# Kernel tuning notes

Measured on AMD Instinct MI355X. Metric: run time of the kernel, lower is better.

Reference implementation:

```python
import jax, jax.numpy as jnp
import numpy as np

D = 128
H = 4
L = 3
MAX_LEN = 696


def _pe(max_len, d):
    pos = jnp.arange(max_len, dtype=jnp.float32)[:, None]
    div = jnp.exp(jnp.arange(0, d, 2, dtype=jnp.float32) * (-jnp.log(jnp.float32(10000.0)) / d))
    pe = jnp.zeros((max_len, d), dtype=jnp.float32)
    pe = pe.at[:, 0::2].set(jnp.sin(pos * div))
    pe = pe.at[:, 1::2].set(jnp.cos(pos * div))
    return pe  # [max_len, d]


def _ln(x, w, b, eps=1e-5):
    m = jnp.mean(x, axis=-1, keepdims=True)
    v = jnp.mean((x - m) ** 2, axis=-1, keepdims=True)
    return (x - m) / jnp.sqrt(v + eps) * w + b


def _mha(xq, xkv, wqkv, bqkv, wo, bo, mask=None):
    # xq: [Tq,B,d], xkv: [Tk,B,d] (seq-first, torch convention)
    d = xq.shape[-1]
    hd = d // H
    q = xq @ wqkv[:d].T + bqkv[:d]
    k = xkv @ wqkv[d:2 * d].T + bqkv[d:2 * d]
    v = xkv @ wqkv[2 * d:].T + bqkv[2 * d:]

    def split(t):
        T, B, _ = t.shape
        return t.reshape(T, B, H, hd).transpose(1, 2, 0, 3)  # [B,H,T,hd]

    qh, kh, vh = split(q), split(k), split(v)
    s = jnp.einsum('bhqd,bhkd->bhqk', qh, kh) / jnp.sqrt(jnp.float32(hd))
    if mask is not None:
        s = jnp.where(mask, jnp.float32(-1e9), s)
    a = jax.nn.softmax(s, axis=-1)
    o = jnp.einsum('bhqk,bhkd->bhqd', a, vh)
    Tq, B = xq.shape[0], xq.shape[1]
    o = o.transpose(2, 0, 1, 3).reshape(Tq, B, d)
    return o @ wo.T + bo


def _forward(src, tgt, emb_in_w, emb_in_b, emb_out_w, emb_out_b,
             enc_qkv_w, enc_qkv_b, enc_proj_w, enc_proj_b,
             enc_ff1_w, enc_ff1_b, enc_ff2_w, enc_ff2_b, enc_ln_w, enc_ln_b,
             dec_sa_qkv_w, dec_sa_qkv_b, dec_sa_proj_w, dec_sa_proj_b,
             dec_ca_qkv_w, dec_ca_qkv_b, dec_ca_proj_w, dec_ca_proj_b,
             dec_ff1_w, dec_ff1_b, dec_ff2_w, dec_ff2_b, dec_ln_w, dec_ln_b,
             head_w, head_b):
    pe = _pe(MAX_LEN, D)
    # ---- encoder ----
    src_p = jnp.transpose(src, (2, 0, 1))  # [S,B,1]
    x = src_p @ emb_in_w.T + emb_in_b + pe[:src_p.shape[0], None, :]
    for i in range(L):
        a = _mha(x, x, enc_qkv_w[i], enc_qkv_b[i], enc_proj_w[i], enc_proj_b[i])
        x = _ln(x + a, enc_ln_w[i, 0], enc_ln_b[i, 0])
        f = jax.nn.relu(x @ enc_ff1_w[i].T + enc_ff1_b[i]) @ enc_ff2_w[i].T + enc_ff2_b[i]
        x = _ln(x + f, enc_ln_w[i, 1], enc_ln_b[i, 1])
    memory = x  # [S,B,D]
    # ---- decoder (full teacher forcing: loop collapses to one causal pass) ----
    tgt_p = jnp.transpose(tgt, (2, 0, 1))  # [T,B,1]
    T = tgt_p.shape[0]
    y = tgt_p[:T - 1] @ emb_out_w.T + emb_out_b  # [T-1,B,D]
    # original code applies pos encoding only to the initial token of the decode loop
    y = y.at[0].add(pe[0])
    mask = jnp.triu(jnp.ones((T - 1, T - 1), dtype=bool), k=1)  # True = masked
    for i in range(L):
        a = _mha(y, y, dec_sa_qkv_w[i], dec_sa_qkv_b[i], dec_sa_proj_w[i], dec_sa_proj_b[i], mask=mask)
        y = _ln(y + a, dec_ln_w[i, 0], dec_ln_b[i, 0])
        c = _mha(y, memory, dec_ca_qkv_w[i], dec_ca_qkv_b[i], dec_ca_proj_w[i], dec_ca_proj_b[i])
        y = _ln(y + c, dec_ln_w[i, 1], dec_ln_b[i, 1])
        f = jax.nn.relu(y @ dec_ff1_w[i].T + dec_ff1_b[i]) @ dec_ff2_w[i].T + dec_ff2_b[i]
        y = _ln(y + f, dec_ln_w[i, 2], dec_ln_b[i, 2])
    out = y @ head_w.T + head_b  # [T-1,B,1]
    return jnp.transpose(out, (1, 2, 0))  # [B,1,T-1]


def setup_inputs() -> dict:
    key = jax.random.key(0)
    ks = iter(jax.random.split(key, 64))

    def n(shape, s=0.02):
        return (jax.random.normal(next(ks), shape) * s).astype(jnp.float32)

    return {
        'src': jax.random.normal(next(ks), (64, 1, 696), dtype=jnp.float32),
        'tgt': jax.random.normal(next(ks), (64, 1, 512), dtype=jnp.float32),
        'emb_in_w': n((D, 1)), 'emb_in_b': n((D,)),
        'emb_out_w': n((D, 1)), 'emb_out_b': n((D,)),
        'enc_qkv_w': n((L, 3 * D, D)), 'enc_qkv_b': n((L, 3 * D)),
        'enc_proj_w': n((L, D, D)), 'enc_proj_b': n((L, D)),
        'enc_ff1_w': n((L, D, D)), 'enc_ff1_b': n((L, D)),
        'enc_ff2_w': n((L, D, D)), 'enc_ff2_b': n((L, D)),
        'enc_ln_w': jnp.ones((L, 2, D), dtype=jnp.float32),
        'enc_ln_b': jnp.zeros((L, 2, D), dtype=jnp.float32),
        'dec_sa_qkv_w': n((L, 3 * D, D)), 'dec_sa_qkv_b': n((L, 3 * D)),
        'dec_sa_proj_w': n((L, D, D)), 'dec_sa_proj_b': n((L, D)),
        'dec_ca_qkv_w': n((L, 3 * D, D)), 'dec_ca_qkv_b': n((L, 3 * D)),
        'dec_ca_proj_w': n((L, D, D)), 'dec_ca_proj_b': n((L, D)),
        'dec_ff1_w': n((L, D, D)), 'dec_ff1_b': n((L, D)),
        'dec_ff2_w': n((L, D, D)), 'dec_ff2_b': n((L, D)),
        'dec_ln_w': jnp.ones((L, 3, D), dtype=jnp.float32),
        'dec_ln_b': jnp.zeros((L, 3, D), dtype=jnp.float32),
        'head_w': n((1, D)), 'head_b': n((1,)),
    }


def reference(src, tgt, emb_in_w, emb_in_b, emb_out_w, emb_out_b,
              enc_qkv_w, enc_qkv_b, enc_proj_w, enc_proj_b,
              enc_ff1_w, enc_ff1_b, enc_ff2_w, enc_ff2_b, enc_ln_w, enc_ln_b,
              dec_sa_qkv_w, dec_sa_qkv_b, dec_sa_proj_w, dec_sa_proj_b,
              dec_ca_qkv_w, dec_ca_qkv_b, dec_ca_proj_w, dec_ca_proj_b,
              dec_ff1_w, dec_ff1_b, dec_ff2_w, dec_ff2_b, dec_ln_w, dec_ln_b,
              head_w, head_b):
    return _forward(src, tgt, emb_in_w, emb_in_b, emb_out_w, emb_out_b,
                    enc_qkv_w, enc_qkv_b, enc_proj_w, enc_proj_b,
                    enc_ff1_w, enc_ff1_b, enc_ff2_w, enc_ff2_b, enc_ln_w, enc_ln_b,
                    dec_sa_qkv_w, dec_sa_qkv_b, dec_sa_proj_w, dec_sa_proj_b,
                    dec_ca_qkv_w, dec_ca_qkv_b, dec_ca_proj_w, dec_ca_proj_b,
                    dec_ff1_w, dec_ff1_b, dec_ff2_w, dec_ff2_b, dec_ln_w, dec_ln_b,
                    head_w, head_b)
```

## Files before the change

kernel.cpp:

```cpp
#include <hip/hip_runtime.h>
#include <hip/hip_bf16.h>


typedef unsigned short u16;
typedef unsigned int u32;
typedef float f32x4 __attribute__((ext_vector_type(4)));
typedef float f32x2 __attribute__((ext_vector_type(2)));
typedef float f32x16 __attribute__((ext_vector_type(16)));
typedef unsigned short u16x8 __attribute__((ext_vector_type(8)));
typedef unsigned int u32x2 __attribute__((ext_vector_type(2)));
typedef unsigned int u32x4 __attribute__((ext_vector_type(4)));
typedef __bf16 bf16x8 __attribute__((ext_vector_type(8)));

static __device__ __forceinline__ float bf2f(u16 u) {
  u32 x = ((u32)u) << 16;
  return __builtin_bit_cast(float, x);
}
static __device__ __forceinline__ u16 f2bf(float f) {
  u32 x = __builtin_bit_cast(u32, f);
  u32 r = (x + 0x7fffu + ((x >> 16) & 1u)) >> 16;
  return (u16)r;
}
static __device__ __forceinline__ f32x4 mfma16(bf16x8 a, bf16x8 b, f32x4 c) {
  return __builtin_amdgcn_mfma_f32_16x16x32_bf16(a, b, c, 0, 0, 0);
}
static __device__ __forceinline__ f32x16 mfma32(bf16x8 a, bf16x8 b, f32x16 c) {
  return __builtin_amdgcn_mfma_f32_32x32x16_bf16(a, b, c, 0, 0, 0);
}
static __device__ __forceinline__ void plswap(u32& a, u32& b) {
  u32x2 r = __builtin_amdgcn_permlane32_swap(a, b, false, false);
  a = r.x; b = r.y;
}

__global__ void detect_k(const u32* __restrict__ ones, int* __restrict__ flag) {
  *flag = (ones[0] == 0x3F803F80u) ? 1 : 0;
}

struct CvtArgs {
  const void* p[32];
  int n[32];
  int off[32];
};

__global__ __launch_bounds__(256) void cvt_all(CvtArgs A, const int* __restrict__ flag,
                                               float* __restrict__ poolf,
                                               u16* __restrict__ poolb) {
  int ti = blockIdx.y;
  int i = blockIdx.x * 256 + threadIdx.x;
  int n = A.n[ti];
  if (i >= n) return;
  int o = A.off[ti] + i;
  if (*flag) {
    u16 raw = ((const u16*)A.p[ti])[i];
    poolb[o] = raw;
    poolf[o] = bf2f(raw);
  } else {
    float v = ((const float*)A.p[ti])[i];
    poolf[o] = v;
    poolb[o] = f2bf(v);
  }
}

__global__ void embed_enc(const float* __restrict__ src, const float* __restrict__ w,
                          const float* __restrict__ b, float* __restrict__ X,
                          u16* __restrict__ Xb) {
  int s = blockIdx.x, d = threadIdx.x;
  float freq = __expf(-(float)(d & 126) * 0.07195578415606394f);
  float arg = (float)s * freq;
  float pe = (d & 1) ? cosf(arg) : sinf(arg);
  float wd = w[d], bd = b[d];
  for (int bb = 0; bb < 64; ++bb) {
    float v = src[bb * 696 + s] * wd + bd + pe;
    size_t o = ((size_t)s * 64 + bb) * 128 + d;
    X[o] = v;
    Xb[o] = f2bf(v);
  }
}

__global__ void embed_dec(const float* __restrict__ tgt, const float* __restrict__ w,
                          const float* __restrict__ b, float* __restrict__ Y,
                          u16* __restrict__ Yb) {
  int tt = blockIdx.x, d = threadIdx.x;
  float wd = w[d], bd = b[d];
  float pe0 = (tt == 0 && (d & 1)) ? 1.0f : 0.0f;
  for (int bb = 0; bb < 64; ++bb) {
    float v = tgt[bb * 512 + tt] * wd + bd + pe0;
    size_t o = ((size_t)tt * 64 + bb) * 128 + d;
    Y[o] = v;
    Yb[o] = f2bf(v);
  }
}

__global__ __launch_bounds__(256) void gemm_ln(
    const u16* __restrict__ Xb, const u16* __restrict__ Wb,
    const float* __restrict__ bias, float* __restrict__ R,
    u16* __restrict__ Rb, const float* __restrict__ lnw,
    const float* __restrict__ lnb) {
  __shared__ u16 Ws[128][136];
  const int t = threadIdx.x;
  const int n0 = blockIdx.x << 6;
  const int wv = t >> 6, lane = t & 63, lg = lane >> 4, lr = lane & 15;
  const int r0 = n0 + (wv << 4);

#pragma unroll
  for (int i = 0; i < 8; ++i) {
    int idx = t + (i << 8);
    int r = idx >> 4, c = (idx & 15) << 3;
    *(u16x8*)&Ws[r][c] = *(const u16x8*)(Wb + ((size_t)r << 7) + c);
  }
  bf16x8 afr[4];
  const int arow = r0 + lr;
#pragma unroll
  for (int ks = 0; ks < 4; ++ks)
    afr[ks] = *(const bf16x8*)(Xb + ((size_t)arow << 7) + (ks << 5) + (lg << 3));
  __syncthreads();

  f32x4 acc[8] = {};
#pragma unroll
  for (int ks = 0; ks < 4; ++ks) {
#pragma unroll
    for (int cb = 0; cb < 8; ++cb) {
      bf16x8 bfr = *(const bf16x8*)&Ws[(cb << 4) + lr][(ks << 5) + (lg << 3)];
      acc[cb] = mfma16(afr[ks], bfr, acc[cb]);
    }
  }

  float vals[8][4];
#pragma unroll
  for (int cb = 0; cb < 8; ++cb) {
    float bv = bias[(cb << 4) + lr];
#pragma unroll
    for (int r = 0; r < 4; ++r) {
      size_t row = (size_t)(r0 + (lg << 2) + r);
      vals[cb][r] = acc[cb][r] + bv + R[(row << 7) + (cb << 4) + lr];
    }
  }
  float mean[4], rstd[4];
#pragma unroll
  for (int r = 0; r < 4; ++r) {
    float s = 0.0f, s2 = 0.0f;
#pragma unroll
    for (int cb = 0; cb < 8; ++cb) {
      float v = vals[cb][r];
      s += v; s2 += v * v;
    }
    s += __shfl_xor(s, 1); s2 += __shfl_xor(s2, 1);
    s += __shfl_xor(s, 2); s2 += __shfl_xor(s2, 2);
    s += __shfl_xor(s, 4); s2 += __shfl_xor(s2, 4);
    s += __shfl_xor(s, 8); s2 += __shfl_xor(s2, 8);
    float m = s * 0.0078125f;
    float var = s2 * 0.0078125f - m * m;
    mean[r] = m;
    rstd[r] = rsqrtf(var + 1e-5f);
  }
#pragma unroll
  for (int cb = 0; cb < 8; ++cb) {
    float w = lnw[(cb << 4) + lr], bb = lnb[(cb << 4) + lr];
#pragma unroll
    for (int r = 0; r < 4; ++r) {
      float v = (vals[cb][r] - mean[r]) * rstd[r] * w + bb;
      size_t o = ((size_t)(r0 + (lg << 2) + r) << 7) + (cb << 4) + lr;
      R[o] = v;
      Rb[o] = f2bf(v);
    }
  }
}

__global__ __launch_bounds__(256) void gemm_ff(
    const u16* __restrict__ Xb, const u16* __restrict__ W1,
    const float* __restrict__ b1, const u16* __restrict__ W2,
    const float* __restrict__ b2, float* __restrict__ R,
    u16* __restrict__ Rb, const float* __restrict__ lnw,
    const float* __restrict__ lnb) {
  __shared__ u16 Ws[128][136];
  __shared__ u16 Hs[64][136];
  const int t = threadIdx.x;
  const int n0 = blockIdx.x << 6;
  const int wv = t >> 6, lane = t & 63, lg = lane >> 4, lr = lane & 15;
  const int r0 = n0 + (wv << 4);

#pragma unroll
  for (int i = 0; i < 8; ++i) {
    int idx = t + (i << 8);
    int r = idx >> 4, c = (idx & 15) << 3;
    *(u16x8*)&Ws[r][c] = *(const u16x8*)(W1 + ((size_t)r << 7) + c);
  }
  bf16x8 afr[4];
  const int arow = r0 + lr;
#pragma unroll
  for (int ks = 0; ks < 4; ++ks)
    afr[ks] = *(const bf16x8*)(Xb + ((size_t)arow << 7) + (ks << 5) + (lg << 3));
  __syncthreads();

  f32x4 acc[8] = {};
#pragma unroll
  for (int ks = 0; ks < 4; ++ks) {
#pragma unroll
    for (int cb = 0; cb < 8; ++cb) {
      bf16x8 bfr = *(const bf16x8*)&Ws[(cb << 4) + lr][(ks << 5) + (lg << 3)];
      acc[cb] = mfma16(afr[ks], bfr, acc[cb]);
    }
  }
#pragma unroll
  for (int cb = 0; cb < 8; ++cb) {
    float bv = b1[(cb << 4) + lr];
#pragma unroll
    for (int r = 0; r < 4; ++r) {
      float v = fmaxf(acc[cb][r] + bv, 0.0f);
      Hs[(wv << 4) + (lg << 2) + r][(cb << 4) + lr] = f2bf(v);
    }
  }
  __syncthreads();

#pragma unroll
  for (int i = 0; i < 8; ++i) {
    int idx = t + (i << 8);
    int r = idx >> 4, c = (idx & 15) << 3;
    *(u16x8*)&Ws[r][c] = *(const u16x8*)(W2 + ((size_t)r << 7) + c);
  }
  __syncthreads();

  bf16x8 hfr[4];
#pragma unroll
  for (int ks = 0; ks < 4; ++ks)
    hfr[ks] = *(const bf16x8*)&Hs[(wv << 4) + lr][(ks << 5) + (lg << 3)];
#pragma unroll
  for (int cb = 0; cb < 8; ++cb) acc[cb] = f32x4{0, 0, 0, 0};
#pragma unroll
  for (int ks = 0; ks < 4; ++ks) {
#pragma unroll
    for (int cb = 0; cb < 8; ++cb) {
      bf16x8 bfr = *(const bf16x8*)&Ws[(cb << 4) + lr][(ks << 5) + (lg << 3)];
      acc[cb] = mfma16(hfr[ks], bfr, acc[cb]);
    }
  }

  float vals[8][4];
#pragma unroll
  for (int cb = 0; cb < 8; ++cb) {
    float bv = b2[(cb << 4) + lr];
#pragma unroll
    for (int r = 0; r < 4; ++r) {
      size_t row = (size_t)(r0 + (lg << 2) + r);
      vals[cb][r] = acc[cb][r] + bv + R[(row << 7) + (cb << 4) + lr];
    }
  }
  float mean[4], rstd[4];
#pragma unroll
  for (int r = 0; r < 4; ++r) {
    float s = 0.0f, s2 = 0.0f;
#pragma unroll
    for (int cb = 0; cb < 8; ++cb) {
      float v = vals[cb][r];
      s += v; s2 += v * v;
    }
    s += __shfl_xor(s, 1); s2 += __shfl_xor(s2, 1);
    s += __shfl_xor(s, 2); s2 += __shfl_xor(s2, 2);
    s += __shfl_xor(s, 4); s2 += __shfl_xor(s2, 4);
    s += __shfl_xor(s, 8); s2 += __shfl_xor(s2, 8);
    float m = s * 0.0078125f;
    float var = s2 * 0.0078125f - m * m;
    mean[r] = m;
    rstd[r] = rsqrtf(var + 1e-5f);
  }
#pragma unroll
  for (int cb = 0; cb < 8; ++cb) {
    float w = lnw[(cb << 4) + lr], bb = lnb[(cb << 4) + lr];
#pragma unroll
    for (int r = 0; r < 4; ++r) {
      float v = (vals[cb][r] - mean[r]) * rstd[r] * w + bb;
      size_t o = ((size_t)(r0 + (lg << 2) + r) << 7) + (cb << 4) + lr;
      R[o] = v;
      Rb[o] = f2bf(v);
    }
  }
}

__global__ __launch_bounds__(256) void gemm_qkv(
    const u16* __restrict__ Xb, const u16* __restrict__ Wb,
    const float* __restrict__ bias, u16* __restrict__ Qg,
    u16* __restrict__ Kg, u16* __restrict__ Vg, int M, int kbase, int vbase) {
  __shared__ u16 Xs[64][136];
  __shared__ u16 Ws[64][136];
  const int t = threadIdx.x;
  const int n0 = blockIdx.x << 6, m0 = blockIdx.y << 6;
  const int wq = t >> 6, lane = t & 63, lg = lane >> 4, lr = lane & 15;
  const int wr = (wq >> 1) << 5, wc = (wq & 1) << 5;
  const float QS = 0.17677669529663687f * 1.4426950408889634f;

#pragma unroll
  for (int i = 0; i < 4; ++i) {
    int idx = t + (i << 8);
    int r = idx >> 4, c = (idx & 15) << 3;
    *(u16x8*)&Xs[r][c] = *(const u16x8*)(Xb + (size_t)(n0 + r) * 128 + c);
    *(u16x8*)&Ws[r][c] = *(const u16x8*)(Wb + (size_t)(m0 + r) * 128 + c);
  }
  __syncthreads();

  f32x4 acc00 = {0,0,0,0}, acc01 = {0,0,0,0}, acc10 = {0,0,0,0}, acc11 = {0,0,0,0};
#pragma unroll
  for (int ks = 0; ks < 4; ++ks) {
    bf16x8 a0 = *(const bf16x8*)&Xs[wr + lr][(ks << 5) + (lg << 3)];
    bf16x8 a1 = *(const bf16x8*)&Xs[wr + 16 + lr][(ks << 5) + (lg << 3)];
    bf16x8 b0 = *(const bf16x8*)&Ws[wc + lr][(ks << 5) + (lg << 3)];
    bf16x8 b1 = *(const bf16x8*)&Ws[wc + 16 + lr][(ks << 5) + (lg << 3)];
    acc00 = mfma16(a0, b0, acc00);
    acc01 = mfma16(a0, b1, acc01);
    acc10 = mfma16(a1, b0, acc10);
    acc11 = mfma16(a1, b1, acc11);
  }

  f32x4 accs[2][2] = {{acc00, acc01}, {acc10, acc11}};
#pragma unroll
  for (int mi = 0; mi < 2; ++mi) {
#pragma unroll
    for (int ni = 0; ni < 2; ++ni) {
      int col = m0 + wc + (ni << 4) + lr;
      float bv = bias[col];
#pragma unroll
      for (int r = 0; r < 4; ++r) {
        int row = n0 + wr + (mi << 4) + (lg << 2) + r;
        float v = accs[mi][ni][r] + bv;
        size_t ro = (size_t)row << 7;
        if (col < kbase) {
          Qg[ro + col] = f2bf(v * QS);
        } else if (col < vbase) {
          Kg[ro + (col - kbase)] = f2bf(v);
        } else {
          Vg[ro + (col - vbase)] = f2bf(v);
        }
      }
    }
  }
}

__global__ __launch_bounds__(256) void attn_g(
    const u16* __restrict__ Qg, const u16* __restrict__ Kg,
    const u16* __restrict__ Vg, u16* __restrict__ Ob,
    int Tq, int Tk, int causal, int bpb) {
  __shared__ u16 Ks[64][44];
  __shared__ u16 Vs[32][74];
  __shared__ float Lw[4][36];
  const int t = threadIdx.x;
  const int wv = t >> 6, lane = t & 63;
  const int lq = lane & 31, hi = lane >> 5;
  const int p = blockIdx.x;
  const int idx = p >> 3;
  const int bh = ((p & 7) << 5) + idx / bpb;
  const int blk = idx % bpb;
  const int nstrips = (Tq + 31) >> 5;
  const int strip = blk * 4 + wv;
  const bool active = strip < nstrips;
  const int b = bh >> 2, h = bh & 3;
  const int qw = (active ? strip : (nstrips - 1)) << 5;

  bf16x8 qf[2];
  {
    int ql = qw + lq; if (ql > Tq - 1) ql = Tq - 1;
    const u16* qp = Qg + (((size_t)ql * 64 + b) << 7) + h * 32 + (hi << 3);
    qf[0] = *(const bf16x8*)qp;
    qf[1] = *(const bf16x8*)(qp + 16);
  }

  f32x16 o = {};
  float lsum = 0.0f;

  const int nfull = causal ? (qw >> 6) : (Tk >> 6);
  int lastcol = causal ? qw + 31 : Tk - 1;
  if (lastcol > Tk - 1) lastcol = Tk - 1;
  int ntiles = (lastcol >> 6) + 1;
  if (!active) ntiles = 0;

  int lastq_blk = blk * 128 + 127;
  if (lastq_blk > Tq - 1) lastq_blk = Tq - 1;
  int lastcol_blk = causal ? lastq_blk : Tk - 1;
  if (lastcol_blk > Tk - 1) lastcol_blk = Tk - 1;
  const int ntb = (lastcol_blk >> 6) + 1;

  const int stok = t >> 2, sc = (t & 3) << 3;

  for (int kt = 0; kt < ntb; ++kt) {
    const int k0 = kt << 6;
    __syncthreads();
    {
      int tok = k0 + stok; if (tok > Tk - 1) tok = Tk - 1;
      size_t roff = (((size_t)tok * 64 + b) << 7) + h * 32 + sc;
      *(u16x8*)&Ks[stok][sc] = *(const u16x8*)(Kg + roff);
      u16x8 vv = *(const u16x8*)(Vg + roff);
#pragma unroll
      for (int e = 0; e < 8; ++e) Vs[sc + e][stok] = vv[e];
    }
    __syncthreads();
    if (kt >= ntiles) continue;
    const bool masked = (kt >= nfull);

#pragma unroll
    for (int kb = 0; kb < 2; ++kb) {
      const int krow = (kb << 5) + lq;
      bf16x8 ka0 = *(const bf16x8*)&Ks[krow][hi << 3];
      bf16x8 ka1 = *(const bf16x8*)&Ks[krow][16 + (hi << 3)];
      f32x16 s = {};
      __builtin_amdgcn_s_setprio(1);
      s = mfma32(ka0, qf[0], s);
      s = mfma32(ka1, qf[1], s);
      __builtin_amdgcn_s_setprio(0);

      float pv[16];
#pragma unroll
      for (int r = 0; r < 16; ++r) {
        float sv = s[r];
        if (masked) {
          int kk = k0 + (kb << 5) + (r & 3) + ((r >> 2) << 3) + (hi << 2);
          int q = qw + lq;
          bool ok = causal ? (kk <= q) : (kk < Tk);
          sv = ok ? sv : -1e30f;
        }
        float e = exp2f(sv);
        pv[r] = e;
        lsum += e;
      }
      u32 u[8];
#pragma unroll
      for (int m = 0; m < 8; ++m)
        asm("v_cvt_pk_bf16_f32 %0, %1, %2" : "=v"(u[m]) : "v"(pv[2 * m]), "v"(pv[2 * m + 1]));

#pragma unroll
      for (int c = 0; c < 2; ++c) {
        u32 a0 = u[4 * c + 0], b0 = u[4 * c + 2];
        u32 a1 = u[4 * c + 1], b1 = u[4 * c + 3];
        plswap(a0, b0);
        plswap(a1, b1);
        u32x4 wv4 = {a0, a1, b0, b1};
        bf16x8 pf = __builtin_bit_cast(bf16x8, wv4);
        bf16x8 vf = *(const bf16x8*)&Vs[lq][(kb << 5) + (c << 4) + (hi << 3)];
        __builtin_amdgcn_s_setprio(1);
        o = mfma32(pf, vf, o);
        __builtin_amdgcn_s_setprio(0);
      }
    }
  }

  if (active) {
    float lt = lsum + __shfl_xor(lsum, 32);
    if (hi == 0) Lw[wv][lq] = 1.0f / lt;
    f32x4 li[4];
#pragma unroll
    for (int g = 0; g < 4; ++g)
      li[g] = *(const f32x4*)&Lw[wv][(hi << 2) + (g << 3)];
#pragma unroll
    for (int r = 0; r < 16; ++r) {
      int q = qw + (r & 3) + ((r >> 2) << 3) + (hi << 2);
      if (q < Tq) {
        Ob[(((size_t)q * 64 + b) << 7) + h * 32 + lq] = f2bf(o[r] * li[r >> 2][r & 3]);
      }
    }
  }
}

__global__ __launch_bounds__(256) void head_k(
    const float* __restrict__ Y, const float* __restrict__ w,
    const float* __restrict__ bh, void* __restrict__ out, const int* __restrict__ flag) {
  int n = (blockIdx.x << 2) + (threadIdx.x >> 6);
  int lane = threadIdx.x & 63;
  const float* yp = Y + (size_t)n * 128 + (lane << 1);
  float s = yp[0] * w[lane << 1] + yp[1] * w[(lane << 1) + 1];
#pragma unroll
  for (int off = 1; off < 64; off <<= 1) s += __shfl_xor(s, off);
  if (lane == 0) {
    int tt = n >> 6, bb = n & 63;
    float r = s + bh[0];
    int idx = bb * 511 + tt;
    if (*flag) ((u16*)out)[idx] = f2bf(r);
    else       ((float*)out)[idx] = r;
  }
}

extern "C" void kernel_launch(void* const* d_in, const int* in_sizes, int n_in,
                              void* d_out, int out_size, void* d_ws, size_t ws_size,
                              hipStream_t stream) {
  (void)out_size; (void)ws_size;
  CvtArgs A;
  long off[33]; off[0] = 0;
  int maxn = 0;
  for (int i = 0; i < 32; ++i) {
    int n = (i < n_in) ? in_sizes[i] : 0;
    A.p[i] = (i < n_in) ? d_in[i] : d_in[0];
    A.n[i] = n;
    A.off[i] = (int)off[i];
    off[i + 1] = off[i] + n;
    if (n > maxn) maxn = n;
  }
  const size_t offA = (size_t)((off[32] + 15) & ~15l);

  const size_t NE = 44544;
  const size_t ND = 32704;
  float* ws   = (float*)d_ws;
  int*   flag = (int*)d_ws;
  float* Wp   = ws + 16;
  float* Xe   = Wp + offA;
  float* Yd   = Xe + NE * 128;
  u16*   U    = (u16*)(Yd + ND * 128);
  u16*   Wb   = U;
  u16*   Xebf = Wb + offA;
  u16*   Ydbf = Xebf + NE * 128;
  u16*   TMPbf= Ydbf + ND * 128;
  u16*   Qgb  = TMPbf + NE * 128;
  u16*   Kgb  = Qgb + NE * 128;
  u16*   Vgb  = Kgb + NE * 128;

  const float* F = Wp;
  detect_k<<<1, 1, 0, stream>>>((const u32*)d_in[14], flag);
  cvt_all<<<dim3((maxn + 255) / 256, 32), 256, 0, stream>>>(A, flag, Wp, Wb);

  embed_enc<<<dim3(696), dim3(128), 0, stream>>>(F + A.off[0], F + A.off[2], F + A.off[3], Xe, Xebf);
  for (int i = 0; i < 3; ++i) {
    gemm_qkv<<<dim3(696, 6), 256, 0, stream>>>(Xebf, Wb + A.off[6] + i * 49152, F + A.off[7] + i * 384,
                                               Qgb, Kgb, Vgb, 384, 128, 256);
    attn_g<<<dim3(1536), 256, 0, stream>>>(Qgb, Kgb, Vgb, TMPbf, 696, 696, 0, 6);
    gemm_ln<<<dim3(696), 256, 0, stream>>>(TMPbf, Wb + A.off[8] + i * 16384, F + A.off[9] + i * 128,
                                           Xe, Xebf, F + A.off[14] + (i * 2 + 0) * 128, F + A.off[15] + (i * 2 + 0) * 128);
    gemm_ff<<<dim3(696), 256, 0, stream>>>(Xebf, Wb + A.off[10] + i * 16384, F + A.off[11] + i * 128,
                                           Wb + A.off[12] + i * 16384, F + A.off[13] + i * 128,
                                           Xe, Xebf, F + A.off[14] + (i * 2 + 1) * 128, F + A.off[15] + (i * 2 + 1) * 128);
  }

  embed_dec<<<dim3(511), dim3(128), 0, stream>>>(F + A.off[1], F + A.off[4], F + A.off[5], Yd, Ydbf);
  for (int i = 0; i < 3; ++i) {
    gemm_qkv<<<dim3(511, 6), 256, 0, stream>>>(Ydbf, Wb + A.off[16] + i * 49152, F + A.off[17] + i * 384,
                                               Qgb, Kgb, Vgb, 384, 128, 256);
    attn_g<<<dim3(1024), 256, 0, stream>>>(Qgb, Kgb, Vgb, TMPbf, 511, 511, 1, 4);
    gemm_ln<<<dim3(511), 256, 0, stream>>>(TMPbf, Wb + A.off[18] + i * 16384, F + A.off[19] + i * 128,
                                           Yd, Ydbf, F + A.off[28] + (i * 3 + 0) * 128, F + A.off[29] + (i * 3 + 0) * 128);
    gemm_qkv<<<dim3(511, 2), 256, 0, stream>>>(Ydbf, Wb + A.off[20] + i * 49152, F + A.off[21] + i * 384,
                                               Qgb, nullptr, nullptr, 128, 128, 128);
    gemm_qkv<<<dim3(696, 4), 256, 0, stream>>>(Xebf, Wb + A.off[20] + i * 49152 + 16384, F + A.off[21] + i * 384 + 128,
                                               nullptr, Kgb, Vgb, 256, 0, 128);
    attn_g<<<dim3(1024), 256, 0, stream>>>(Qgb, Kgb, Vgb, TMPbf, 511, 696, 0, 4);
    gemm_ln<<<dim3(511), 256, 0, stream>>>(TMPbf, Wb + A.off[22] + i * 16384, F + A.off[23] + i * 128,
                                           Yd, Ydbf, F + A.off[28] + (i * 3 + 1) * 128, F + A.off[29] + (i * 3 + 1) * 128);
    gemm_ff<<<dim3(511), 256, 0, stream>>>(Ydbf, Wb + A.off[24] + i * 16384, F + A.off[25] + i * 128,
                                           Wb + A.off[26] + i * 16384, F + A.off[27] + i * 128,
                                           Yd, Ydbf, F + A.off[28] + (i * 3 + 2) * 128, F + A.off[29] + (i * 3 + 2) * 128);
  }

  head_k<<<dim3(8176), 256, 0, stream>>>(Yd, F + A.off[30], F + A.off[31], d_out, flag);
}
```

Before: 823.8 us.

## Fuse attention with output projection, residual add and LayerNorm

Replaces the separate attention and gemm_ln kernels with one kernel. Each block handles one batch element and a 64-query strip across all four heads, one head per wave. After normalising, the block writes the attention output to shared memory and runs the output projection, residual add and LayerNorm in place. This removes the bf16 intermediate round trip through global memory and one launch per attention layer. In exchange there are fewer blocks (704 and 512 instead of 1536 and 1024), larger shared-memory use and more work per block, which can lower occupancy and load balance, especially on the causal path.

```diff
diff --git a/kernel.cpp b/kernel.cpp
--- a/kernel.cpp
+++ b/kernel.cpp
@@ -91,81 +91,6 @@
   }
 }
 
-__global__ __launch_bounds__(256) void gemm_ln(
-    const u16* __restrict__ Xb, const u16* __restrict__ Wb,
-    const float* __restrict__ bias, float* __restrict__ R,
-    u16* __restrict__ Rb, const float* __restrict__ lnw,
-    const float* __restrict__ lnb) {
-  __shared__ u16 Ws[128][136];
-  const int t = threadIdx.x;
-  const int n0 = blockIdx.x << 6;
-  const int wv = t >> 6, lane = t & 63, lg = lane >> 4, lr = lane & 15;
-  const int r0 = n0 + (wv << 4);
-
-#pragma unroll
-  for (int i = 0; i < 8; ++i) {
-    int idx = t + (i << 8);
-    int r = idx >> 4, c = (idx & 15) << 3;
-    *(u16x8*)&Ws[r][c] = *(const u16x8*)(Wb + ((size_t)r << 7) + c);
-  }
-  bf16x8 afr[4];
-  const int arow = r0 + lr;
-#pragma unroll
-  for (int ks = 0; ks < 4; ++ks)
-    afr[ks] = *(const bf16x8*)(Xb + ((size_t)arow << 7) + (ks << 5) + (lg << 3));
-  __syncthreads();
-
-  f32x4 acc[8] = {};
-#pragma unroll
-  for (int ks = 0; ks < 4; ++ks) {
-#pragma unroll
-    for (int cb = 0; cb < 8; ++cb) {
-      bf16x8 bfr = *(const bf16x8*)&Ws[(cb << 4) + lr][(ks << 5) + (lg << 3)];
-      acc[cb] = mfma16(afr[ks], bfr, acc[cb]);
-    }
-  }
-
-  float vals[8][4];
-#pragma unroll
-  for (int cb = 0; cb < 8; ++cb) {
-    float bv = bias[(cb << 4) + lr];
-#pragma unroll
-    for (int r = 0; r < 4; ++r) {
-      size_t row = (size_t)(r0 + (lg << 2) + r);
-      vals[cb][r] = acc[cb][r] + bv + R[(row << 7) + (cb << 4) + lr];
-    }
-  }
-  float mean[4], rstd[4];
-#pragma unroll
-  for (int r = 0; r < 4; ++r) {
-    float s = 0.0f, s2 = 0.0f;
-#pragma unroll
-    for (int cb = 0; cb < 8; ++cb) {
-      float v = vals[cb][r];
-      s += v; s2 += v * v;
-    }
-    s += __shfl_xor(s, 1); s2 += __shfl_xor(s2, 1);
-    s += __shfl_xor(s, 2); s2 += __shfl_xor(s2, 2);
-    s += __shfl_xor(s, 4); s2 += __shfl_xor(s2, 4);
-    s += __shfl_xor(s, 8); s2 += __shfl_xor(s2, 8);
-    float m = s * 0.0078125f;
-    float var = s2 * 0.0078125f - m * m;
-    mean[r] = m;
-    rstd[r] = rsqrtf(var + 1e-5f);
-  }
-#pragma unroll
-  for (int cb = 0; cb < 8; ++cb) {
-    float w = lnw[(cb << 4) + lr], bb = lnb[(cb << 4) + lr];
-#pragma unroll
-    for (int r = 0; r < 4; ++r) {
-      float v = (vals[cb][r] - mean[r]) * rstd[r] * w + bb;
-      size_t o = ((size_t)(r0 + (lg << 2) + r) << 7) + (cb << 4) + lr;
-      R[o] = v;
-      Rb[o] = f2bf(v);
-    }
-  }
-}
-
 __global__ __launch_bounds__(256) void gemm_ff(
     const u16* __restrict__ Xb, const u16* __restrict__ W1,
     const float* __restrict__ b1, const u16* __restrict__ W2,
@@ -334,125 +259,197 @@
   }
 }
 
-__global__ __launch_bounds__(256) void attn_g(
+__global__ __launch_bounds__(256) void attn_pl(
     const u16* __restrict__ Qg, const u16* __restrict__ Kg,
-    const u16* __restrict__ Vg, u16* __restrict__ Ob,
-    int Tq, int Tk, int causal, int bpb) {
-  __shared__ u16 Ks[64][44];
-  __shared__ u16 Vs[32][74];
-  __shared__ float Lw[4][36];
+    const u16* __restrict__ Vg, const u16* __restrict__ Wp,
+    const float* __restrict__ bp, float* __restrict__ R,
+    u16* __restrict__ Rb, const float* __restrict__ lnw,
+    const float* __restrict__ lnb, int Tq, int Tk, int causal, int nstrips) {
+  __shared__ u16 KOs[64][132];
+  __shared__ u16 Vs[128][70];
+  __shared__ u16 Ws[64][132];
+  __shared__ float Lw[4][2][36];
   const int t = threadIdx.x;
   const int wv = t >> 6, lane = t & 63;
   const int lq = lane & 31, hi = lane >> 5;
+  const int lr16 = lane & 15, lg16 = lane >> 4;
+  const int h = wv;
   const int p = blockIdx.x;
   const int idx = p >> 3;
-  const int bh = ((p & 7) << 5) + idx / bpb;
-  const int blk = idx % bpb;
-  const int nstrips = (Tq + 31) >> 5;
-  const int strip = blk * 4 + wv;
-  const bool active = strip < nstrips;
-  const int b = bh >> 2, h = bh & 3;
-  const int qw = (active ? strip : (nstrips - 1)) << 5;
-
-  bf16x8 qf[2];
-  {
-    int ql = qw + lq; if (ql > Tq - 1) ql = Tq - 1;
+  const int b = ((p & 7) << 3) + idx / nstrips;
+  const int strip = idx % nstrips;
+  const int q0 = strip << 6;
+
+  bf16x8 qf[2][2];
+#pragma unroll
+  for (int ss = 0; ss < 2; ++ss) {
+    int ql = q0 + (ss << 5) + lq; if (ql > Tq - 1) ql = Tq - 1;
     const u16* qp = Qg + (((size_t)ql * 64 + b) << 7) + h * 32 + (hi << 3);
-    qf[0] = *(const bf16x8*)qp;
-    qf[1] = *(const bf16x8*)(qp + 16);
-  }
-
-  f32x16 o = {};
-  float lsum = 0.0f;
-
-  const int nfull = causal ? (qw >> 6) : (Tk >> 6);
-  int lastcol = causal ? qw + 31 : Tk - 1;
-  if (lastcol > Tk - 1) lastcol = Tk - 1;
-  int ntiles = (lastcol >> 6) + 1;
-  if (!active) ntiles = 0;
-
-  int lastq_blk = blk * 128 + 127;
-  if (lastq_blk > Tq - 1) lastq_blk = Tq - 1;
-  int lastcol_blk = causal ? lastq_blk : Tk - 1;
-  if (lastcol_blk > Tk - 1) lastcol_blk = Tk - 1;
-  const int ntb = (lastcol_blk >> 6) + 1;
-
-  const int stok = t >> 2, sc = (t & 3) << 3;
+    qf[ss][0] = *(const bf16x8*)qp;
+    qf[ss][1] = *(const bf16x8*)(qp + 16);
+  }
+
+  f32x16 o[2] = {};
+  float lsum[2] = {0.0f, 0.0f};
+
+  const int ntb = causal ? (strip + 1) : (((Tk - 1) >> 6) + 1);
 
   for (int kt = 0; kt < ntb; ++kt) {
     const int k0 = kt << 6;
     __syncthreads();
-    {
-      int tok = k0 + stok; if (tok > Tk - 1) tok = Tk - 1;
-      size_t roff = (((size_t)tok * 64 + b) << 7) + h * 32 + sc;
-      *(u16x8*)&Ks[stok][sc] = *(const u16x8*)(Kg + roff);
-      u16x8 vv = *(const u16x8*)(Vg + roff);
-#pragma unroll
-      for (int e = 0; e < 8; ++e) Vs[sc + e][stok] = vv[e];
+#pragma unroll
+    for (int i = 0; i < 4; ++i) {
+      int sidx = t + (i << 8);
+      int row = sidx >> 4, c8 = (sidx & 15) << 3;
+      int tok = k0 + row; if (tok > Tk - 1) tok = Tk - 1;
+      size_t base = (((size_t)tok * 64 + b) << 7) + c8;
+      *(u16x8*)&KOs[row][c8] = *(const u16x8*)(Kg + base);
+      u16x8 vv = *(const u16x8*)(Vg + base);
+#pragma unroll
+      for (int e = 0; e < 8; ++e) Vs[c8 + e][row] = vv[e];
     }
     __syncthreads();
-    if (kt >= ntiles) continue;
-    const bool masked = (kt >= nfull);
-
-#pragma unroll
-    for (int kb = 0; kb < 2; ++kb) {
-      const int krow = (kb << 5) + lq;
-      bf16x8 ka0 = *(const bf16x8*)&Ks[krow][hi << 3];
-      bf16x8 ka1 = *(const bf16x8*)&Ks[krow][16 + (hi << 3)];
-      f32x16 s = {};
-      __builtin_amdgcn_s_setprio(1);
-      s = mfma32(ka0, qf[0], s);
-      s = mfma32(ka1, qf[1], s);
-      __builtin_amdgcn_s_setprio(0);
-
-      float pv[16];
-#pragma unroll
-      for (int r = 0; r < 16; ++r) {
-        float sv = s[r];
-        if (masked) {
-          int kk = k0 + (kb << 5) + (r & 3) + ((r >> 2) << 3) + (hi << 2);
-          int q = qw + lq;
-          bool ok = causal ? (kk <= q) : (kk < Tk);
-          sv = ok ? sv : -1e30f;
+
+#pragma unroll
+    for (int ss = 0; ss < 2; ++ss) {
+      const int qs = q0 + (ss << 5);
+      if (qs >= Tq) continue;
+      int lastc = causal ? qs + 31 : Tk - 1;
+      if (lastc > Tk - 1) lastc = Tk - 1;
+      if (kt > (lastc >> 6)) continue;
+      const int nfull = causal ? (qs >> 6) : (Tk >> 6);
+      const bool masked = (kt >= nfull);
+
+#pragma unroll
+      for (int kb = 0; kb < 2; ++kb) {
+        const int krow = (kb << 5) + lq;
+        bf16x8 ka0 = *(const bf16x8*)&KOs[krow][h * 32 + (hi << 3)];
+        bf16x8 ka1 = *(const bf16x8*)&KOs[krow][h * 32 + 16 + (hi << 3)];
+        f32x16 s = {};
+        __builtin_amdgcn_s_setprio(1);
+        s = mfma32(ka0, qf[ss][0], s);
+        s = mfma32(ka1, qf[ss][1], s);
+        __builtin_amdgcn_s_setprio(0);
+
+        float pvv[16];
+#pragma unroll
+        for (int r = 0; r < 16; ++r) {
+          float sv = s[r];
+          if (masked) {
+            int kk = k0 + (kb << 5) + (r & 3) + ((r >> 2) << 3) + (hi << 2);
+            int q = qs + lq;
+            bool ok = causal ? (kk <= q) : (kk < Tk);
+            sv = ok ? sv : -1e30f;
+          }
+          float e = exp2f(sv);
+          pvv[r] = e;
+          lsum[ss] += e;
         }
-        float e = exp2f(sv);
-        pv[r] = e;
-        lsum += e;
+        u32 u[8];
+#pragma unroll
+        for (int m = 0; m < 8; ++m)
+          asm("v_cvt_pk_bf16_f32 %0, %1, %2" : "=v"(u[m]) : "v"(pvv[2 * m]), "v"(pvv[2 * m + 1]));
+
+#pragma unroll
+        for (int c = 0; c < 2; ++c) {
+          u32 a0 = u[4 * c + 0], b0 = u[4 * c + 2];
+          u32 a1 = u[4 * c + 1], b1 = u[4 * c + 3];
+          plswap(a0, b0);
+          plswap(a1, b1);
+          u32x4 wv4 = {a0, a1, b0, b1};
+          bf16x8 pf = __builtin_bit_cast(bf16x8, wv4);
+          bf16x8 vf = *(const bf16x8*)&Vs[h * 32 + lq][(kb << 5) + (c << 4) + (hi << 3)];
+          __builtin_amdgcn_s_setprio(1);
+          o[ss] = mfma32(pf, vf, o[ss]);
+          __builtin_amdgcn_s_setprio(0);
+        }
       }
-      u32 u[8];
-#pragma unroll
-      for (int m = 0; m < 8; ++m)
-        asm("v_cvt_pk_bf16_f32 %0, %1, %2" : "=v"(u[m]) : "v"(pv[2 * m]), "v"(pv[2 * m + 1]));
-
-#pragma unroll
-      for (int c = 0; c < 2; ++c) {
-        u32 a0 = u[4 * c + 0], b0 = u[4 * c + 2];
-        u32 a1 = u[4 * c + 1], b1 = u[4 * c + 3];
-        plswap(a0, b0);
-        plswap(a1, b1);
-        u32x4 wv4 = {a0, a1, b0, b1};
-        bf16x8 pf = __builtin_bit_cast(bf16x8, wv4);
-        bf16x8 vf = *(const bf16x8*)&Vs[lq][(kb << 5) + (c << 4) + (hi << 3)];
-        __builtin_amdgcn_s_setprio(1);
-        o = mfma32(pf, vf, o);
-        __builtin_amdgcn_s_setprio(0);
+    }
+  }
+
+#pragma unroll
+  for (int ss = 0; ss < 2; ++ss) {
+    float lt = lsum[ss] + __shfl_xor(lsum[ss], 32);
+    if (hi == 0) Lw[wv][ss][lq] = lt > 0.0f ? 1.0f / lt : 0.0f;
+  }
+  __syncthreads();
+
+#pragma unroll
+  for (int ss = 0; ss < 2; ++ss) {
+    f32x4 li[4];
+#pragma unroll
+    for (int g = 0; g < 4; ++g)
+      li[g] = *(const f32x4*)&Lw[wv][ss][(hi << 2) + (g << 3)];
+#pragma unroll
+    for (int r = 0; r < 16; ++r) {
+      int qrow = (ss << 5) + (r & 3) + ((r >> 2) << 3) + (hi << 2);
+      KOs[qrow][h * 32 + lq] = f2bf(o[ss][r] * li[r >> 2][r & 3]);
+    }
+  }
+
+  float vals[2][4][4];
+#pragma unroll
+  for (int ch = 0; ch < 2; ++ch) {
+    __syncthreads();
+#pragma unroll
+    for (int i = 0; i < 4; ++i) {
+      int sidx = t + (i << 8);
+      int row = sidx >> 4, c8 = (sidx & 15) << 3;
+      *(u16x8*)&Ws[row][c8] = *(const u16x8*)(Wp + ((size_t)((ch << 6) + row) << 7) + c8);
+    }
+    __syncthreads();
+
+    f32x4 acc[4] = {};
+#pragma unroll
+    for (int ks = 0; ks < 4; ++ks) {
+      bf16x8 af = *(const bf16x8*)&KOs[(wv << 4) + lr16][(ks << 5) + (lg16 << 3)];
+#pragma unroll
+      for (int cb = 0; cb < 4; ++cb) {
+        bf16x8 bf = *(const bf16x8*)&Ws[(cb << 4) + lr16][(ks << 5) + (lg16 << 3)];
+        acc[cb] = mfma16(af, bf, acc[cb]);
       }
     }
-  }
-
-  if (active) {
-    float lt = lsum + __shfl_xor(lsum, 32);
-    if (hi == 0) Lw[wv][lq] = 1.0f / lt;
-    f32x4 li[4];
-#pragma unroll
-    for (int g = 0; g < 4; ++g)
-      li[g] = *(const f32x4*)&Lw[wv][(hi << 2) + (g << 3)];
-#pragma unroll
-    for (int r = 0; r < 16; ++r) {
-      int q = qw + (r & 3) + ((r >> 2) << 3) + (hi << 2);
-      if (q < Tq) {
-        Ob[(((size_t)q * 64 + b) << 7) + h * 32 + lq] = f2bf(o[r] * li[r >> 2][r & 3]);
+#pragma unroll
+    for (int cb = 0; cb < 4; ++cb) {
+      int col = (ch << 6) + (cb << 4) + lr16;
+      float bv = bp[col];
+#pragma unroll
+      for (int r = 0; r < 4; ++r) {
+        int q = q0 + (wv << 4) + (lg16 << 2) + r;
+        int qc = q > Tq - 1 ? Tq - 1 : q;
+        vals[ch][cb][r] = acc[cb][r] + bv + R[(((size_t)qc * 64 + b) << 7) + col];
       }
+    }
+  }
+
+#pragma unroll
+  for (int r = 0; r < 4; ++r) {
+    float s = 0.0f, s2 = 0.0f;
+#pragma unroll
+    for (int ch = 0; ch < 2; ++ch)
+#pragma unroll
+      for (int cb = 0; cb < 4; ++cb) {
+        float v = vals[ch][cb][r];
+        s += v; s2 += v * v;
+      }
+    s += __shfl_xor(s, 1); s2 += __shfl_xor(s2, 1);
+    s += __shfl_xor(s, 2); s2 += __shfl_xor(s2, 2);
+    s += __shfl_xor(s, 4); s2 += __shfl_xor(s2, 4);
+    s += __shfl_xor(s, 8); s2 += __shfl_xor(s2, 8);
+    float m = s * 0.0078125f;
+    float rstd = rsqrtf(s2 * 0.0078125f - m * m + 1e-5f);
+    int q = q0 + (wv << 4) + (lg16 << 2) + r;
+    if (q < Tq) {
+      size_t base = (((size_t)q * 64 + b) << 7);
+#pragma unroll
+      for (int ch = 0; ch < 2; ++ch)
+#pragma unroll
+        for (int cb = 0; cb < 4; ++cb) {
+          int col = (ch << 6) + (cb << 4) + lr16;
+          float v = (vals[ch][cb][r] - m) * rstd * lnw[col] + lnb[col];
+          R[base + col] = v;
+          Rb[base + col] = f2bf(v);
+        }
     }
   }
 }
@@ -503,8 +500,7 @@
   u16*   Wb   = U;
   u16*   Xebf = Wb + offA;
   u16*   Ydbf = Xebf + NE * 128;
-  u16*   TMPbf= Ydbf + ND * 128;
-  u16*   Qgb  = TMPbf + NE * 128;
+  u16*   Qgb  = Ydbf + ND * 128;
   u16*   Kgb  = Qgb + NE * 128;
   u16*   Vgb  = Kgb + NE * 128;
 
@@ -516,9 +512,11 @@
   for (int i = 0; i < 3; ++i) {
     gemm_qkv<<<dim3(696, 6), 256, 0, stream>>>(Xebf, Wb + A.off[6] + i * 49152, F + A.off[7] + i * 384,
                                                Qgb, Kgb, Vgb, 384, 128, 256);
-    attn_g<<<dim3(1536), 256, 0, stream>>>(Qgb, Kgb, Vgb, TMPbf, 696, 696, 0, 6);
-    gemm_ln<<<dim3(696), 256, 0, stream>>>(TMPbf, Wb + A.off[8] + i * 16384, F + A.off[9] + i * 128,
-                                           Xe, Xebf, F + A.off[14] + (i * 2 + 0) * 128, F + A.off[15] + (i * 2 + 0) * 128);
+    attn_pl<<<dim3(704), 256, 0, stream>>>(Qgb, Kgb, Vgb,
+                                           Wb + A.off[8] + i * 16384, F + A.off[9] + i * 128,
+                                           Xe, Xebf,
+                                           F + A.off[14] + (i * 2 + 0) * 128, F + A.off[15] + (i * 2 + 0) * 128,
+                                           696, 696, 0, 11);
     gemm_ff<<<dim3(696), 256, 0, stream>>>(Xebf, Wb + A.off[10] + i * 16384, F + A.off[11] + i * 128,
                                            Wb + A.off[12] + i * 16384, F + A.off[13] + i * 128,
                                            Xe, Xebf, F + A.off[14] + (i * 2 + 1) * 128, F + A.off[15] + (i * 2 + 1) * 128);
@@ -528,16 +526,20 @@
   for (int i = 0; i < 3; ++i) {
     gemm_qkv<<<dim3(511, 6), 256, 0, stream>>>(Ydbf, Wb + A.off[16] + i * 49152, F + A.off[17] + i * 384,
                                                Qgb, Kgb, Vgb, 384, 128, 256);
-    attn_g<<<dim3(1024), 256, 0, stream>>>(Qgb, Kgb, Vgb, TMPbf, 511, 511, 1, 4);
-    gemm_ln<<<dim3(511), 256, 0, stream>>>(TMPbf, Wb + A.off[18] + i * 16384, F + A.off[19] + i * 128,
-                                           Yd, Ydbf, F + A.off[28] + (i * 3 + 0) * 128, F + A.off[29] + (i * 3 + 0) * 128);
+    attn_pl<<<dim3(512), 256, 0, stream>>>(Qgb, Kgb, Vgb,
+                                           Wb + A.off[18] + i * 16384, F + A.off[19] + i * 128,
+                                           Yd, Ydbf,
+                                           F + A.off[28] + (i * 3 + 0) * 128, F + A.off[29] + (i * 3 + 0) * 128,
+                                           511, 511, 1, 8);
     gemm_qkv<<<dim3(511, 2), 256, 0, stream>>>(Ydbf, Wb + A.off[20] + i * 49152, F + A.off[21] + i * 384,
                                                Qgb, nullptr, nullptr, 128, 128, 128);
     gemm_qkv<<<dim3(696, 4), 256, 0, stream>>>(Xebf, Wb + A.off[20] + i * 49152 + 16384, F + A.off[21] + i * 384 + 128,
                                                nullptr, Kgb, Vgb, 256, 0, 128);
-    attn_g<<<dim3(1024), 256, 0, stream>>>(Qgb, Kgb, Vgb, TMPbf, 511, 696, 0, 4);
-    gemm_ln<<<dim3(511), 256, 0, stream>>>(TMPbf, Wb + A.off[22] + i * 16384, F + A.off[23] + i * 128,
-                                           Yd, Ydbf, F + A.off[28] + (i * 3 + 1) * 128, F + A.off[29] + (i * 3 + 1) * 128);
+    attn_pl<<<dim3(512), 256, 0, stream>>>(Qgb, Kgb, Vgb,
+                                           Wb + A.off[22] + i * 16384, F + A.off[23] + i * 128,
+                                           Yd, Ydbf,
+                                           F + A.off[28] + (i * 3 + 1) * 128, F + A.off[29] + (i * 3 + 1) * 128,
+                                           511, 696, 0, 8);
     gemm_ff<<<dim3(511), 256, 0, stream>>>(Ydbf, Wb + A.off[24] + i * 16384, F + A.off[25] + i * 128,
                                            Wb + A.off[26] + i * 16384, F + A.off[27] + i * 128,
                                            Yd, Ydbf, F + A.off[28] + (i * 3 + 2) * 128, F + A.off[29] + (i * 3 + 2) * 128);
```

After: 809.4 us. No clear change (-1.7%).
